# Optimization experiments

Hardware: AMD Instinct MI355X
Metric: run time of the kernel (lower is better)

The kernel has to match this reference:

```python
import jax, jax.numpy as jnp
import numpy as np
import math

N, S, C, K, V = 32, 4096, 1, 512, 128
TARGET_SCALE = 0.06  # normalize_scale == embedding_scale when normalize=True


def setup_inputs() -> dict:
    key = jax.random.key(0)
    k1, k2 = jax.random.split(key)
    x0 = jax.random.normal(k1, (N, S, C, V), dtype=jnp.float32)
    emb = jax.random.normal(k2, (C, K, V), dtype=jnp.float32) * TARGET_SCALE
    # after_update(): renormalize each code vector to norm = embedding_scale*sqrt(V)
    tn = TARGET_SCALE * math.sqrt(V)
    emb = emb * (tn / jnp.linalg.norm(emb, axis=2, keepdims=True))
    return {"x0": x0, "embedding0": emb}


def _vq_forward(x0, embedding0):
    tn = TARGET_SCALE * math.sqrt(V)
    # normalize inputs and codebook to the same norm (normalize=True path)
    x = tn * x0 / jnp.linalg.norm(x0, axis=3, keepdims=True)              # (N,S,C,V)
    emb = tn * embedding0 / jnp.linalg.norm(embedding0, axis=2, keepdims=True)  # (C,K,V)

    xf = x.reshape(N * S, C, V)
    x2 = jnp.sum(xf * xf, axis=2)                     # (NS, C)
    e2 = jnp.sum(emb * emb, axis=2)                   # (C, K)
    dots = jnp.einsum('ncv,ckv->nck', xf, emb)        # (NS, C, K)
    d2 = x2[:, :, None] + e2[None, :, :] - 2.0 * dots
    index = jnp.argmin(d2, axis=2)                    # (NS, C) int

    # entropy of code usage: histc over n_classes, normalized by len(index)=NS
    hist = jnp.zeros((K,), jnp.float32).at[index.reshape(-1)].add(1.0)
    prob = hist / float(N * S)
    entropy = -jnp.sum(jnp.where(hist > 0, prob * jnp.log(jnp.where(hist > 0, prob, 1.0)), 0.0))

    # gather selected code vectors per channel
    output = emb[jnp.arange(C)[None, :], index]       # (NS, C, V)
    output = output.reshape(x.shape)                  # (N,S,C,V)

    sg = jax.lax.stop_gradient
    out0 = sg(output - x) + x                                              # straight-through
    out1 = jnp.sum((sg(x) - output) ** 2, axis=3)                          # codebook loss (N,S,C)
    out2 = jnp.sum((x - sg(output)) ** 2, axis=3) + jnp.sum((x - x0) ** 2, axis=3)  # commitment + norm penalty
    return out0, out1, out2, entropy


def reference(x0, embedding0):
    return _vq_forward(x0, embedding0)
```

## Files before the change

### kernel.cpp

```cpp
#include <hip/hip_runtime.h>
#include <math.h>

#define VDIM   128
#define KCODES 512
#define NROWS  (32 * 4096)
#define TILE_ROWS 256
#define TN 0.67882250993908565f

typedef __attribute__((ext_vector_type(8))) short bf16x8;
typedef __attribute__((ext_vector_type(4))) float f32x4;

__device__ __forceinline__ unsigned short f2bf(float f) {
    unsigned u = __float_as_uint(f);
    unsigned r = u + 0x7FFFu + ((u >> 16) & 1u);
    return (unsigned short)(r >> 16);
}

__device__ __forceinline__ bf16x8 pack8(float4 a, float4 b) {
    bf16x8 v;
    v[0] = (short)f2bf(a.x); v[1] = (short)f2bf(a.y);
    v[2] = (short)f2bf(a.z); v[3] = (short)f2bf(a.w);
    v[4] = (short)f2bf(b.x); v[5] = (short)f2bf(b.y);
    v[6] = (short)f2bf(b.z); v[7] = (short)f2bf(b.w);
    return v;
}

__global__ void prep_emb(const float* __restrict__ emb0,
                         float* __restrict__ embn,
                         unsigned short* __restrict__ ebf,
                         float* __restrict__ e2) {
    int k = blockIdx.x;
    int l = threadIdx.x;
    const float* row = emb0 + (size_t)k * VDIM;
    float a = row[l];
    float b = row[l + 64];
    float ss = a * a + b * b;
    #pragma unroll
    for (int off = 32; off; off >>= 1) ss += __shfl_xor(ss, off);
    float nrm = sqrtf(ss);
    float ea = (TN * a) / nrm;
    float eb = (TN * b) / nrm;
    embn[(size_t)k * VDIM + l]      = ea;
    embn[(size_t)k * VDIM + l + 64] = eb;
    ebf[(size_t)k * VDIM + l]      = f2bf(ea);
    ebf[(size_t)k * VDIM + l + 64] = f2bf(eb);
    float s2 = ea * ea + eb * eb;
    #pragma unroll
    for (int off = 32; off; off >>= 1) s2 += __shfl_xor(s2, off);
    if (l == 0) e2[k] = s2;
}

__global__ __launch_bounds__(256) void vq_main(
        const float* __restrict__ x0,
        const unsigned short* __restrict__ ebf,
        const float* __restrict__ embn,
        const float* __restrict__ e2,
        unsigned* __restrict__ hist,
        float* __restrict__ out0,
        float* __restrict__ out1,
        float* __restrict__ out2) {
    int t = threadIdx.x;
    int w = t >> 6;
    int l = t & 63;
    int n15 = l & 15;
    int q = l >> 4;

    int rowbase = blockIdx.x * TILE_ROWS + (w << 6);
    bf16x8 afr[4][4];
    float nsq[4];
    #pragma unroll
    for (int s = 0; s < 4; ++s) {
        const float* xrow = x0 + (size_t)(rowbase + (s << 4) + n15) * VDIM + (q << 3);
        float p0 = 0.f, p1 = 0.f;
        #pragma unroll
        for (int kc = 0; kc < 4; ++kc) {
            const float4* xp = (const float4*)(xrow + (kc << 5));
            float4 a = xp[0], b = xp[1];
            p0 = fmaf(a.x, a.x, p0); p1 = fmaf(a.y, a.y, p1);
            p0 = fmaf(a.z, a.z, p0); p1 = fmaf(a.w, a.w, p1);
            p0 = fmaf(b.x, b.x, p0); p1 = fmaf(b.y, b.y, p1);
            p0 = fmaf(b.z, b.z, p0); p1 = fmaf(b.w, b.w, p1);
            afr[s][kc] = pack8(a, b);
        }
        nsq[s] = p0 + p1;
    }
    #pragma unroll
    for (int s = 0; s < 4; ++s) {
        nsq[s] += __shfl_xor(nsq[s], 16, 64);
        nsq[s] += __shfl_xor(nsq[s], 32, 64);
    }

    float best[4][4];
    int   bidx[4][4];
    #pragma unroll
    for (int s = 0; s < 4; ++s)
        #pragma unroll
        for (int r = 0; r < 4; ++r) { best[s][r] = -3.4e38f; bidx[s][r] = 0; }

    const f32x4 zero4 = {0.f, 0.f, 0.f, 0.f};
    const bf16x8* eb8 = (const bf16x8*)ebf;
    for (int cn = 0; cn < 32; ++cn) {
        int n = (cn << 4) | n15;
        const bf16x8* bp = eb8 + (size_t)n * 16 + q;
        bf16x8 b0 = bp[0], b1 = bp[4], b2 = bp[8], b3 = bp[12];
        #pragma unroll
        for (int s = 0; s < 4; ++s) {
            f32x4 acc = __builtin_amdgcn_mfma_f32_16x16x32_bf16(afr[s][0], b0, zero4, 0, 0, 0);
            acc = __builtin_amdgcn_mfma_f32_16x16x32_bf16(afr[s][1], b1, acc, 0, 0, 0);
            acc = __builtin_amdgcn_mfma_f32_16x16x32_bf16(afr[s][2], b2, acc, 0, 0, 0);
            acc = __builtin_amdgcn_mfma_f32_16x16x32_bf16(afr[s][3], b3, acc, 0, 0, 0);
            #pragma unroll
            for (int r = 0; r < 4; ++r) {
                float d = acc[r];
                if (d > best[s][r]) { best[s][r] = d; bidx[s][r] = n; }
            }
        }
    }

    #pragma unroll
    for (int m = 1; m <= 8; m <<= 1) {
        #pragma unroll
        for (int s = 0; s < 4; ++s)
            #pragma unroll
            for (int r = 0; r < 4; ++r) {
                float ov = __shfl_xor(best[s][r], m, 64);
                int   oi = __shfl_xor(bidx[s][r], m, 64);
                if (ov > best[s][r] || (ov == best[s][r] && oi < bidx[s][r])) {
                    best[s][r] = ov; bidx[s][r] = oi;
                }
            }
    }

    __shared__ int   sbesti[TILE_ROWS];
    __shared__ float sdot[TILE_ROWS];
    __shared__ float sn0[TILE_ROWS];
    if (n15 == 0) {
        #pragma unroll
        for (int s = 0; s < 4; ++s)
            #pragma unroll
            for (int r = 0; r < 4; ++r) {
                int lr = (w << 6) + (s << 4) + (q << 2) + r;
                sbesti[lr] = bidx[s][r];
                sdot[lr]   = best[s][r];
            }
    }
    if (q == 0) {
        #pragma unroll
        for (int s = 0; s < 4; ++s) sn0[(w << 6) + (s << 4) + n15] = nsq[s];
    }
    __syncthreads();

    {
        int lr = t;
        size_t row = (size_t)blockIdx.x * TILE_ROWS + lr;
        int bi = sbesti[lr];
        float dotv = sdot[lr];
        float nn = sn0[lr];
        float sc = TN / sqrtf(nn);
        const float4* ep4 = (const float4*)(embn + (size_t)bi * VDIM);
        float4* op4 = (float4*)(out0 + row * (size_t)VDIM);
        #pragma unroll
        for (int i = 0; i < 32; ++i) op4[i] = ep4[i];
        float o1 = TN * TN + e2[bi] - 2.f * sc * dotv;
        out1[row] = o1;
        float sm = sc - 1.f;
        out2[row] = o1 + sm * sm * nn;
        atomicAdd(&hist[bi], 1u);
    }
}

__global__ void entropy_k(const unsigned* __restrict__ hist,
                          float* __restrict__ out) {
    __shared__ float red[8];
    int t = threadIdx.x;
    float h = (float)hist[t];
    float p = h / (float)NROWS;
    float term = (h > 0.f) ? p * logf(p) : 0.f;
    #pragma unroll
    for (int off = 32; off; off >>= 1) term += __shfl_xor(term, off);
    if ((t & 63) == 0) red[t >> 6] = term;
    __syncthreads();
    if (t == 0) {
        float ssum = 0.f;
        #pragma unroll
        for (int i = 0; i < 8; i++) ssum += red[i];
        out[0] = -ssum;
    }
}

extern "C" void kernel_launch(void* const* d_in, const int* in_sizes, int n_in,
                              void* d_out, int out_size, void* d_ws, size_t ws_size,
                              hipStream_t stream) {
    const float* x0   = (const float*)d_in[0];
    const float* emb0 = (const float*)d_in[1];

    float* embn = (float*)d_ws;
    float* e2   = embn + (size_t)KCODES * VDIM;
    unsigned* hist = (unsigned*)(e2 + KCODES);
    unsigned short* ebf = (unsigned short*)(hist + KCODES);

    float* out  = (float*)d_out;
    float* out0 = out;
    float* out1 = out0 + (size_t)NROWS * VDIM;
    float* out2 = out1 + NROWS;
    float* oent = out2 + NROWS;

    hipMemsetAsync(hist, 0, KCODES * sizeof(unsigned), stream);
    prep_emb<<<KCODES, 64, 0, stream>>>(emb0, embn, ebf, e2);
    vq_main<<<NROWS / TILE_ROWS, 256, 0, stream>>>(x0, ebf, embn, e2, hist,
                                                   out0, out1, out2);
    entropy_k<<<1, KCODES, 0, stream>>>(hist, oent);
}
```

Before: 194.0 us.

## Halve row tile, double-buffer codebook loads, and coalesce output row copies

Halves rows per block (each wave now handles 32 rows with 2 MFMA row-groups instead of 4) and adds a launch-bounds occupancy hint, which doubles the grid and lowers register pressure. The codebook fragment loads are double-buffered so the next chunk's loads are in flight while the current chunk's MFMAs and argmax run. The out0 gather/copy is restructured so 32 lanes cooperatively write one 512-byte row per pass, giving coalesced stores instead of each thread writing a whole row. In exchange, each codebook fragment is reused across fewer rows per wave, so codebook load traffic per row roughly doubles.

```diff
diff --git a/kernel.cpp b/kernel.cpp
--- a/kernel.cpp
+++ b/kernel.cpp
@@ -4,7 +4,7 @@
 #define VDIM   128
 #define KCODES 512
 #define NROWS  (32 * 4096)
-#define TILE_ROWS 256
+#define TILE_ROWS 128
 #define TN 0.67882250993908565f
 
 typedef __attribute__((ext_vector_type(8))) short bf16x8;
@@ -50,7 +50,7 @@
     if (l == 0) e2[k] = s2;
 }
 
-__global__ __launch_bounds__(256) void vq_main(
+__global__ __launch_bounds__(256, 4) void vq_main(
         const float* __restrict__ x0,
         const unsigned short* __restrict__ ebf,
         const float* __restrict__ embn,
@@ -65,11 +65,11 @@
     int n15 = l & 15;
     int q = l >> 4;
 
-    int rowbase = blockIdx.x * TILE_ROWS + (w << 6);
-    bf16x8 afr[4][4];
-    float nsq[4];
-    #pragma unroll
-    for (int s = 0; s < 4; ++s) {
+    int rowbase = blockIdx.x * TILE_ROWS + (w << 5);
+    bf16x8 afr[2][4];
+    float nsq[2];
+    #pragma unroll
+    for (int s = 0; s < 2; ++s) {
         const float* xrow = x0 + (size_t)(rowbase + (s << 4) + n15) * VDIM + (q << 3);
         float p0 = 0.f, p1 = 0.f;
         #pragma unroll
@@ -83,44 +83,64 @@
             afr[s][kc] = pack8(a, b);
         }
         nsq[s] = p0 + p1;
-    }
-    #pragma unroll
-    for (int s = 0; s < 4; ++s) {
         nsq[s] += __shfl_xor(nsq[s], 16, 64);
         nsq[s] += __shfl_xor(nsq[s], 32, 64);
     }
 
-    float best[4][4];
-    int   bidx[4][4];
-    #pragma unroll
-    for (int s = 0; s < 4; ++s)
+    float best[2][4];
+    int   bidx[2][4];
+    #pragma unroll
+    for (int s = 0; s < 2; ++s)
         #pragma unroll
         for (int r = 0; r < 4; ++r) { best[s][r] = -3.4e38f; bidx[s][r] = 0; }
 
     const f32x4 zero4 = {0.f, 0.f, 0.f, 0.f};
     const bf16x8* eb8 = (const bf16x8*)ebf;
-    for (int cn = 0; cn < 32; ++cn) {
-        int n = (cn << 4) | n15;
-        const bf16x8* bp = eb8 + (size_t)n * 16 + q;
-        bf16x8 b0 = bp[0], b1 = bp[4], b2 = bp[8], b3 = bp[12];
-        #pragma unroll
-        for (int s = 0; s < 4; ++s) {
-            f32x4 acc = __builtin_amdgcn_mfma_f32_16x16x32_bf16(afr[s][0], b0, zero4, 0, 0, 0);
-            acc = __builtin_amdgcn_mfma_f32_16x16x32_bf16(afr[s][1], b1, acc, 0, 0, 0);
-            acc = __builtin_amdgcn_mfma_f32_16x16x32_bf16(afr[s][2], b2, acc, 0, 0, 0);
-            acc = __builtin_amdgcn_mfma_f32_16x16x32_bf16(afr[s][3], b3, acc, 0, 0, 0);
-            #pragma unroll
-            for (int r = 0; r < 4; ++r) {
-                float d = acc[r];
-                if (d > best[s][r]) { best[s][r] = d; bidx[s][r] = n; }
-            }
+    const bf16x8* bp0 = eb8 + (size_t)n15 * 16 + q;
+
+    bf16x8 ba[4], bb[4];
+    ba[0] = bp0[0]; ba[1] = bp0[4]; ba[2] = bp0[8]; ba[3] = bp0[12];
+
+#define PROCESS(BUF, CN)                                                        \
+    do {                                                                        \
+        int n_ = ((CN) << 4) | n15;                                             \
+        _Pragma("unroll")                                                       \
+        for (int s = 0; s < 2; ++s) {                                           \
+            f32x4 acc = __builtin_amdgcn_mfma_f32_16x16x32_bf16(                \
+                afr[s][0], BUF[0], zero4, 0, 0, 0);                             \
+            acc = __builtin_amdgcn_mfma_f32_16x16x32_bf16(                      \
+                afr[s][1], BUF[1], acc, 0, 0, 0);                               \
+            acc = __builtin_amdgcn_mfma_f32_16x16x32_bf16(                      \
+                afr[s][2], BUF[2], acc, 0, 0, 0);                               \
+            acc = __builtin_amdgcn_mfma_f32_16x16x32_bf16(                      \
+                afr[s][3], BUF[3], acc, 0, 0, 0);                               \
+            _Pragma("unroll")                                                   \
+            for (int r = 0; r < 4; ++r) {                                       \
+                float d = acc[r];                                               \
+                if (d > best[s][r]) { best[s][r] = d; bidx[s][r] = n_; }        \
+            }                                                                   \
+        }                                                                       \
+    } while (0)
+
+    for (int cn = 0; cn < 32; cn += 2) {
+        {
+            const bf16x8* bp = eb8 + ((size_t)(((cn + 1) << 4) | n15)) * 16 + q;
+            bb[0] = bp[0]; bb[1] = bp[4]; bb[2] = bp[8]; bb[3] = bp[12];
         }
-    }
+        PROCESS(ba, cn);
+        {
+            int cnn = cn + 2 < 32 ? cn + 2 : 31;
+            const bf16x8* bp = eb8 + ((size_t)((cnn << 4) | n15)) * 16 + q;
+            ba[0] = bp[0]; ba[1] = bp[4]; ba[2] = bp[8]; ba[3] = bp[12];
+        }
+        PROCESS(bb, cn + 1);
+    }
+#undef PROCESS
 
     #pragma unroll
     for (int m = 1; m <= 8; m <<= 1) {
         #pragma unroll
-        for (int s = 0; s < 4; ++s)
+        for (int s = 0; s < 2; ++s)
             #pragma unroll
             for (int r = 0; r < 4; ++r) {
                 float ov = __shfl_xor(best[s][r], m, 64);
@@ -136,31 +156,36 @@
     __shared__ float sn0[TILE_ROWS];
     if (n15 == 0) {
         #pragma unroll
-        for (int s = 0; s < 4; ++s)
+        for (int s = 0; s < 2; ++s)
             #pragma unroll
             for (int r = 0; r < 4; ++r) {
-                int lr = (w << 6) + (s << 4) + (q << 2) + r;
+                int lr = (w << 5) + (s << 4) + (q << 2) + r;
                 sbesti[lr] = bidx[s][r];
                 sdot[lr]   = best[s][r];
             }
     }
     if (q == 0) {
         #pragma unroll
-        for (int s = 0; s < 4; ++s) sn0[(w << 6) + (s << 4) + n15] = nsq[s];
+        for (int s = 0; s < 2; ++s) sn0[(w << 5) + (s << 4) + n15] = nsq[s];
     }
     __syncthreads();
 
-    {
-        int lr = t;
-        size_t row = (size_t)blockIdx.x * TILE_ROWS + lr;
+    size_t blockrow = (size_t)blockIdx.x * TILE_ROWS;
+    #pragma unroll
+    for (int pass = 0; pass < 16; ++pass) {
+        int lr = (pass << 3) + (t >> 5);
+        int v4 = t & 31;
         int bi = sbesti[lr];
-        float dotv = sdot[lr];
-        float nn = sn0[lr];
+        float4 e = ((const float4*)(embn + (size_t)bi * VDIM))[v4];
+        ((float4*)(out0 + (blockrow + lr) * (size_t)VDIM))[v4] = e;
+    }
+
+    if (t < TILE_ROWS) {
+        size_t row = blockrow + t;
+        int bi = sbesti[t];
+        float dotv = sdot[t];
+        float nn = sn0[t];
         float sc = TN / sqrtf(nn);
-        const float4* ep4 = (const float4*)(embn + (size_t)bi * VDIM);
-        float4* op4 = (float4*)(out0 + row * (size_t)VDIM);
-        #pragma unroll
-        for (int i = 0; i < 32; ++i) op4[i] = ep4[i];
         float o1 = TN * TN + e2[bi] - 2.f * sc * dotv;
         out1[row] = o1;
         float sm = sc - 1.f;
```

Result: slower. 202.0 us (+4.1%).
